# Optimization experiments

Measured on AMD Instinct MI355X. Metric: run time of the kernel, lower is better.

The kernel has to match this reference:

```python
import math
import jax, jax.numpy as jnp
import numpy as np

NUM_BUCKETS = 32
MAX_DISTANCE = 128


def _relative_position_bucket(relative_position):
    # bidirectional=False: positive relative positions map to bucket 0
    rp = -jnp.minimum(relative_position, 0)  # non-negative distances
    max_exact = NUM_BUCKETS // 2
    is_small = rp < max_exact
    # clamp to >=1 before log to avoid log(0); those lanes are selected away by is_small
    rp_large = max_exact + (
        jnp.log(jnp.maximum(rp, 1).astype(jnp.float32) / max_exact)
        / math.log(MAX_DISTANCE / max_exact)
        * (NUM_BUCKETS - max_exact)
    ).astype(jnp.int32)
    rp_large = jnp.minimum(rp_large, NUM_BUCKETS - 1)
    return jnp.where(is_small, rp, rp_large)


def setup_inputs() -> dict:
    key = jax.random.key(0)
    k1, k2, k3, k4 = jax.random.split(key, 4)
    B, L, H, E = 4, 2048, 8, 64
    return {
        "queries": jax.random.normal(k1, (B, L, H, E), dtype=jnp.float32),
        "keys": jax.random.normal(k2, (B, L, H, E), dtype=jnp.float32),
        "values": jax.random.normal(k3, (B, L, H, E), dtype=jnp.float32),
        "bias_table": jax.random.normal(k4, (NUM_BUCKETS, 8), dtype=jnp.float32),
    }


def reference(queries, keys, values, bias_table):
    B, L, H, E = queries.shape
    scale = 1.0 / math.sqrt(E)

    # scores: [B, H, L, S]
    scores = jnp.einsum("blhe,bshe->bhls", queries, keys)

    # causal mask (TriangularCausalMask): masked positions -> -inf BEFORE scaling
    causal = jnp.triu(jnp.ones((L, L), dtype=bool), k=1)  # [L, L]
    scores = jnp.where(causal[None, None], -jnp.inf, scores)

    attn = scale * scores

    # T5-style relative position bias: [1, H, L, L]
    pos = jnp.arange(L)
    rel_pos = pos[None, :] - pos[:, None]  # memory - query
    buckets = _relative_position_bucket(rel_pos)  # [L, L] in [0, 32)
    bias = bias_table[buckets]  # [L, L, 8]
    bias = jnp.transpose(bias, (2, 0, 1))[None]  # [1, 8, L, L]
    attn = attn + bias

    series = jax.nn.softmax(attn, axis=-1)  # dropout p=0.0 -> identity
    V = jnp.einsum("bhls,bshd->blhd", series, values)
    return V
```

## Files before the change

kernel.cpp:

```cpp
#include <hip/hip_runtime.h>
#include <hip/hip_bf16.h>
#include <math.h>

typedef __attribute__((ext_vector_type(8)))  short short8;
typedef __attribute__((ext_vector_type(4)))  float floatx4;
typedef __attribute__((ext_vector_type(16))) float f32x16;

#define L_SEQ 2048
#define NHEADS 8
#define EDIM 64
#define PLANE (L_SEQ * EDIM)
#define LOG2E 1.4426950408889634f

union U8 { unsigned u[4]; short8 s; };

__device__ __forceinline__ unsigned cvt_pk(float lo, float hi) {
    unsigned r;
    asm("v_cvt_pk_bf16_f32 %0, %1, %2" : "=v"(r) : "v"(lo), "v"(hi));
    return r;
}
__device__ __forceinline__ short8 pack8(floatx4 a, floatx4 b) {
    U8 r;
    r.u[0] = cvt_pk(a[0], a[1]); r.u[1] = cvt_pk(a[2], a[3]);
    r.u[2] = cvt_pk(b[0], b[1]); r.u[3] = cvt_pk(b[2], b[3]);
    return r.s;
}
__device__ __forceinline__ unsigned xswap32(unsigned v) {
    return (unsigned)__shfl_xor((int)v, 32);
}

__global__ __launch_bounds__(256) void prep_frag(
    const float* __restrict__ K, const float* __restrict__ V,
    unsigned short* __restrict__ Kf, unsigned short* __restrict__ Vf)
{
    __shared__ unsigned short Tk[64][72];
    __shared__ unsigned short Tv[64][72];
    const int st  = blockIdx.x;
    const int bh  = blockIdx.y;
    const int b   = bh >> 3, h = bh & 7;
    const int tid = threadIdx.x;
    const int sb  = st * 64;

    {
        int s0 = tid >> 3, e0 = (tid & 7) * 8;
        #pragma unroll
        for (int j = 0; j < 2; ++j) {
            int s = s0 + j * 32;
            const float* kp = K + ((size_t)(b * L_SEQ + sb + s) * NHEADS + h) * EDIM + e0;
            floatx4 f0 = *(const floatx4*)kp;
            floatx4 f1 = *(const floatx4*)(kp + 4);
            *(short8*)&Tk[s][e0] = pack8(f0, f1);
        }
    }
    {
        int e = tid & 63, sg = tid >> 6;
        #pragma unroll
        for (int j = 0; j < 16; ++j) {
            int s = sg * 16 + j;
            float v = V[((size_t)(b * L_SEQ + sb + s) * NHEADS + h) * EDIM + e];
            union { float f; unsigned u; } cv; cv.f = v;
            Tv[e][s] = (unsigned short)((cv.u + 0x7FFFu + ((cv.u >> 16) & 1u)) >> 16);
        }
    }
    __syncthreads();
    {
        int s2 = tid >> 7, t7 = tid & 127, ec = t7 >> 5, l31 = t7 & 31;
        #pragma unroll
        for (int hi = 0; hi < 2; ++hi) {
            int row = s2 * 32 + l31, e = ec * 16 + hi * 8;
            short8 v = *(const short8*)&Tk[row][e];
            size_t unit = (((size_t)bh * 64 + st * 2 + s2) * 4 + ec) * 64 + hi * 32 + l31;
            *(short8*)&Kf[unit * 8] = v;
        }
    }
    {
        int s2 = tid >> 7, t7 = tid & 127, et = t7 >> 6, lane = t7 & 63;
        #pragma unroll
        for (int c = 0; c < 2; ++c) {
            int e = et * 32 + (lane & 31), k0 = s2 * 32 + c * 16 + (lane >> 5) * 8;
            short8 v = *(const short8*)&Tv[e][k0];
            size_t unit = ((((size_t)bh * 64 + st * 2 + s2) * 2 + et) * 2 + c) * 64 + lane;
            *(short8*)&Vf[unit * 8] = v;
        }
    }
}

__global__ __launch_bounds__(256, 3) void attn_fwd(
    const float* __restrict__ Q, const unsigned short* __restrict__ Kf,
    const unsigned short* __restrict__ Vf, const float* __restrict__ table,
    float* __restrict__ Out)
{
    __shared__ __align__(16) float bias_lds[L_SEQ];
    __shared__ __align__(16) float osc[2][32][64];
    __shared__ float lsc[2][64];

    const int bid = blockIdx.x;
    const int wid = (bid & 7) * 256 + (bid >> 3);
    const int bh  = wid >> 6;
    const int qg  = 63 - (wid & 63);
    const int b    = bh >> 3, h = bh & 7;
    const int tid  = threadIdx.x;
    const int w    = tid >> 6, lane = tid & 63;
    const int q32  = lane & 31;
    const int hi   = lane >> 5;
    const int hi4  = 4 * hi, hi8 = 8 * hi;
    const int qs   = qg * 32;
    const int qrow = qs + q32;
    const int nsub = qg + 1;

    const int dmax = nsub * 32;
    for (int d = tid; d < dmax; d += 256) {
        int bucket;
        if (d < 16) bucket = d;
        else {
            float t = logf((float)d * 0.0625f) / 2.0794415416798357f * 16.0f;
            int bb = 16 + (int)t;
            bucket = bb < 31 ? bb : 31;
        }
        bias_lds[d] = table[bucket * NHEADS + h] * LOG2E;
    }

    const float* qptr = Q + ((size_t)(b * L_SEQ + qrow) * NHEADS + h) * EDIM;
    short8 qfrag[4];
    #pragma unroll
    for (int ec = 0; ec < 4; ++ec) {
        floatx4 f0 = *(const floatx4*)(qptr + ec * 16 + hi8);
        floatx4 f1 = *(const floatx4*)(qptr + ec * 16 + hi8 + 4);
        qfrag[ec] = pack8(f0, f1);
    }
    __syncthreads();

    const int len = (nsub + 3) >> 2;
    const int r0  = w * len;
    const int r1  = (r0 + len < nsub) ? r0 + len : nsub;

    const unsigned short* kfb = Kf + (size_t)bh * PLANE + lane * 8;
    const unsigned short* vfb = Vf + (size_t)bh * PLANE + lane * 8;

    float  l_run = 0.f;
    f32x16 o_acc[2] = {};

    const float qscale = 0.125f * LOG2E;
    for (int s32 = r0; s32 < r1; ++s32) {
        const bool diag = (s32 == qg);
        const int  kv0s = s32 * 32;

        const unsigned short* kp = kfb + (size_t)s32 * 2048;
        const unsigned short* vp = vfb + (size_t)s32 * 2048;
        short8 kf0 = *(const short8*)(kp);
        short8 kf1 = *(const short8*)(kp + 512);
        short8 kf2 = *(const short8*)(kp + 1024);
        short8 kf3 = *(const short8*)(kp + 1536);
        short8 vf0 = *(const short8*)(vp);
        short8 vf1 = *(const short8*)(vp + 512);
        short8 vf2 = *(const short8*)(vp + 1024);
        short8 vf3 = *(const short8*)(vp + 1536);

        f32x16 st = {};
        __builtin_amdgcn_s_setprio(1);
        st = __builtin_amdgcn_mfma_f32_32x32x16_bf16(kf0, qfrag[0], st, 0, 0, 0);
        st = __builtin_amdgcn_mfma_f32_32x32x16_bf16(kf1, qfrag[1], st, 0, 0, 0);
        st = __builtin_amdgcn_mfma_f32_32x32x16_bf16(kf2, qfrag[2], st, 0, 0, 0);
        st = __builtin_amdgcn_mfma_f32_32x32x16_bf16(kf3, qfrag[3], st, 0, 0, 0);
        __builtin_amdgcn_s_setprio(0);

        float p[16];
        if (!diag) {
            const float* bptr = &bias_lds[qrow - kv0s - hi4];
            #pragma unroll
            for (int r = 0; r < 16; ++r)
                p[r] = exp2f(fmaf(qscale, st[r], bptr[-(r & 3) - 8 * (r >> 2)]));
        } else {
            #pragma unroll
            for (int r = 0; r < 16; ++r) {
                int kidx = (r & 3) + 8 * (r >> 2) + hi4;
                int d = q32 - kidx;
                int dc = d < 0 ? 0 : d;
                float ex = exp2f(fmaf(qscale, st[r], bias_lds[dc]));
                p[r] = (d >= 0) ? ex : 0.0f;
            }
        }

        float s8[8], s4[4], s2[2];
        #pragma unroll
        for (int i = 0; i < 8; ++i) s8[i] = p[2*i] + p[2*i+1];
        #pragma unroll
        for (int i = 0; i < 4; ++i) s4[i] = s8[2*i] + s8[2*i+1];
        s2[0] = s4[0] + s4[1]; s2[1] = s4[2] + s4[3];
        float tsum = s2[0] + s2[1];
        l_run += tsum + __shfl_xor(tsum, 32);

        unsigned a0 = cvt_pk(p[0],  p[1]),  b0 = cvt_pk(p[2],  p[3]);
        unsigned c0 = cvt_pk(p[4],  p[5]),  d0 = cvt_pk(p[6],  p[7]);
        unsigned a1 = cvt_pk(p[8],  p[9]),  b1 = cvt_pk(p[10], p[11]);
        unsigned c1 = cvt_pk(p[12], p[13]), d1 = cvt_pk(p[14], p[15]);
        unsigned as0 = xswap32(a0), bs0 = xswap32(b0);
        unsigned cs0 = xswap32(c0), ds0 = xswap32(d0);
        unsigned as1 = xswap32(a1), bs1 = xswap32(b1);
        unsigned cs1 = xswap32(c1), ds1 = xswap32(d1);
        U8 pf0;
        pf0.u[0] = hi ? cs0 : a0;
        pf0.u[1] = hi ? ds0 : b0;
        pf0.u[2] = hi ? c0  : as0;
        pf0.u[3] = hi ? d0  : bs0;
        U8 pf1;
        pf1.u[0] = hi ? cs1 : a1;
        pf1.u[1] = hi ? ds1 : b1;
        pf1.u[2] = hi ? c1  : as1;
        pf1.u[3] = hi ? d1  : bs1;

        __builtin_amdgcn_s_setprio(1);
        o_acc[0] = __builtin_amdgcn_mfma_f32_32x32x16_bf16(pf0.s, vf0, o_acc[0], 0, 0, 0);
        o_acc[0] = __builtin_amdgcn_mfma_f32_32x32x16_bf16(pf1.s, vf1, o_acc[0], 0, 0, 0);
        o_acc[1] = __builtin_amdgcn_mfma_f32_32x32x16_bf16(pf0.s, vf2, o_acc[1], 0, 0, 0);
        o_acc[1] = __builtin_amdgcn_mfma_f32_32x32x16_bf16(pf1.s, vf3, o_acc[1], 0, 0, 0);
        __builtin_amdgcn_s_setprio(0);
    }

    __syncthreads();
    if (w & 1) {
        int slot = w >> 1;
        #pragma unroll
        for (int et = 0; et < 2; ++et)
            #pragma unroll
            for (int r = 0; r < 16; ++r)
                osc[slot][et * 16 + r][lane] = o_acc[et][r];
        lsc[slot][lane] = l_run;
    }
    __syncthreads();
    if (!(w & 1)) {
        int slot = w >> 1;
        l_run += lsc[slot][lane];
        #pragma unroll
        for (int et = 0; et < 2; ++et)
            #pragma unroll
            for (int r = 0; r < 16; ++r)
                o_acc[et][r] += osc[slot][et * 16 + r][lane];
    }
    __syncthreads();
    if (w == 2) {
        #pragma unroll
        for (int et = 0; et < 2; ++et)
            #pragma unroll
            for (int r = 0; r < 16; ++r)
                osc[0][et * 16 + r][lane] = o_acc[et][r];
        lsc[0][lane] = l_run;
    }
    __syncthreads();
    if (w == 0) {
        l_run += lsc[0][lane];
        #pragma unroll
        for (int et = 0; et < 2; ++et)
            #pragma unroll
            for (int r = 0; r < 16; ++r)
                o_acc[et][r] += osc[0][et * 16 + r][lane];

        float inv = 1.0f / l_run;
        #pragma unroll
        for (int r = 0; r < 16; ++r) {
            int qv = (r & 3) + 8 * (r >> 2) + hi4;
            float iv = __shfl(inv, qv);
            float* op = Out + ((size_t)(b * L_SEQ + qs + qv) * NHEADS + h) * EDIM + q32;
            op[0]  = o_acc[0][r] * iv;
            op[32] = o_acc[1][r] * iv;
        }
    }
}

extern "C" void kernel_launch(void* const* d_in, const int* in_sizes, int n_in,
                              void* d_out, int out_size, void* d_ws, size_t ws_size,
                              hipStream_t stream) {
    const float* Q     = (const float*)d_in[0];
    const float* K     = (const float*)d_in[1];
    const float* V     = (const float*)d_in[2];
    const float* table = (const float*)d_in[3];
    float* Out = (float*)d_out;
    unsigned short* Kf = (unsigned short*)d_ws;
    unsigned short* Vf = Kf + (size_t)4 * NHEADS * PLANE;
    (void)in_sizes; (void)n_in; (void)out_size; (void)ws_size;

    dim3 pgrid(32, 32);
    prep_frag<<<pgrid, 256, 0, stream>>>(K, V, Kf, Vf);
    attn_fwd<<<dim3(2048), 256, 0, stream>>>(Q, Kf, Vf, table, Out);
}
```

Measured before the change: 58.47 us.

## Compute softmax row sums via MFMA with ones and use permlane32 swap

Replaces the scalar tree reduction and cross-half shuffle of the softmax denominator with two extra MFMAs that multiply the bf16 probability fragments by a ones matrix, so row sums land in the same layout as the output accumulator. It also replaces the eight ds_swizzle/shfl_xor exchanges plus selects with four v_permlane32_swap instructions to build the P fragments. The final normalization no longer needs a lane shuffle. The trade-offs are extra matrix work per tile and more accumulator registers, and the denominator is now summed from bf16-rounded probabilities.

New measurement: 58.75 us. Within noise of the previous version (+0.5%).

```diff
diff --git a/kernel.cpp b/kernel.cpp
--- a/kernel.cpp
+++ b/kernel.cpp
@@ -24,9 +24,6 @@
     r.u[0] = cvt_pk(a[0], a[1]); r.u[1] = cvt_pk(a[2], a[3]);
     r.u[2] = cvt_pk(b[0], b[1]); r.u[3] = cvt_pk(b[2], b[3]);
     return r.s;
-}
-__device__ __forceinline__ unsigned xswap32(unsigned v) {
-    return (unsigned)__shfl_xor((int)v, 32);
 }
 
 __global__ __launch_bounds__(256) void prep_frag(
@@ -92,7 +89,7 @@
 {
     __shared__ __align__(16) float bias_lds[L_SEQ];
     __shared__ __align__(16) float osc[2][32][64];
-    __shared__ float lsc[2][64];
+    __shared__ float lsc[2][2][16];
 
     const int bid = blockIdx.x;
     const int wid = (bid & 7) * 256 + (bid >> 3);
@@ -137,8 +134,12 @@
     const unsigned short* kfb = Kf + (size_t)bh * PLANE + lane * 8;
     const unsigned short* vfb = Vf + (size_t)bh * PLANE + lane * 8;
 
-    float  l_run = 0.f;
+    U8 onesf;
+    onesf.u[0] = 0x3F803F80u; onesf.u[1] = 0x3F803F80u;
+    onesf.u[2] = 0x3F803F80u; onesf.u[3] = 0x3F803F80u;
+
     f32x16 o_acc[2] = {};
+    f32x16 o_l = {};
 
     const float qscale = 0.125f * LOG2E;
     for (int s32 = r0; s32 < r1; ++s32) {
@@ -181,39 +182,26 @@
             }
         }
 
-        float s8[8], s4[4], s2[2];
-        #pragma unroll
-        for (int i = 0; i < 8; ++i) s8[i] = p[2*i] + p[2*i+1];
-        #pragma unroll
-        for (int i = 0; i < 4; ++i) s4[i] = s8[2*i] + s8[2*i+1];
-        s2[0] = s4[0] + s4[1]; s2[1] = s4[2] + s4[3];
-        float tsum = s2[0] + s2[1];
-        l_run += tsum + __shfl_xor(tsum, 32);
-
-        unsigned a0 = cvt_pk(p[0],  p[1]),  b0 = cvt_pk(p[2],  p[3]);
-        unsigned c0 = cvt_pk(p[4],  p[5]),  d0 = cvt_pk(p[6],  p[7]);
-        unsigned a1 = cvt_pk(p[8],  p[9]),  b1 = cvt_pk(p[10], p[11]);
-        unsigned c1 = cvt_pk(p[12], p[13]), d1 = cvt_pk(p[14], p[15]);
-        unsigned as0 = xswap32(a0), bs0 = xswap32(b0);
-        unsigned cs0 = xswap32(c0), ds0 = xswap32(d0);
-        unsigned as1 = xswap32(a1), bs1 = xswap32(b1);
-        unsigned cs1 = xswap32(c1), ds1 = xswap32(d1);
+        unsigned x0 = cvt_pk(p[0],  p[1]),  x1 = cvt_pk(p[2],  p[3]);
+        unsigned y0 = cvt_pk(p[4],  p[5]),  y1 = cvt_pk(p[6],  p[7]);
+        unsigned x2 = cvt_pk(p[8],  p[9]),  x3 = cvt_pk(p[10], p[11]);
+        unsigned y2 = cvt_pk(p[12], p[13]), y3 = cvt_pk(p[14], p[15]);
+        asm("v_permlane32_swap_b32 %0, %1" : "+v"(x0), "+v"(y0));
+        asm("v_permlane32_swap_b32 %0, %1" : "+v"(x1), "+v"(y1));
+        asm("v_permlane32_swap_b32 %0, %1" : "+v"(x2), "+v"(y2));
+        asm("v_permlane32_swap_b32 %0, %1" : "+v"(x3), "+v"(y3));
         U8 pf0;
-        pf0.u[0] = hi ? cs0 : a0;
-        pf0.u[1] = hi ? ds0 : b0;
-        pf0.u[2] = hi ? c0  : as0;
-        pf0.u[3] = hi ? d0  : bs0;
+        pf0.u[0] = x0; pf0.u[1] = x1; pf0.u[2] = y0; pf0.u[3] = y1;
         U8 pf1;
-        pf1.u[0] = hi ? cs1 : a1;
-        pf1.u[1] = hi ? ds1 : b1;
-        pf1.u[2] = hi ? c1  : as1;
-        pf1.u[3] = hi ? d1  : bs1;
+        pf1.u[0] = x2; pf1.u[1] = x3; pf1.u[2] = y2; pf1.u[3] = y3;
 
         __builtin_amdgcn_s_setprio(1);
         o_acc[0] = __builtin_amdgcn_mfma_f32_32x32x16_bf16(pf0.s, vf0, o_acc[0], 0, 0, 0);
         o_acc[0] = __builtin_amdgcn_mfma_f32_32x32x16_bf16(pf1.s, vf1, o_acc[0], 0, 0, 0);
         o_acc[1] = __builtin_amdgcn_mfma_f32_32x32x16_bf16(pf0.s, vf2, o_acc[1], 0, 0, 0);
         o_acc[1] = __builtin_amdgcn_mfma_f32_32x32x16_bf16(pf1.s, vf3, o_acc[1], 0, 0, 0);
+        o_l      = __builtin_amdgcn_mfma_f32_32x32x16_bf16(pf0.s, onesf.s, o_l, 0, 0, 0);
+        o_l      = __builtin_amdgcn_mfma_f32_32x32x16_bf16(pf1.s, onesf.s, o_l, 0, 0, 0);
         __builtin_amdgcn_s_setprio(0);
     }
 
@@ -225,17 +213,21 @@
             #pragma unroll
             for (int r = 0; r < 16; ++r)
                 osc[slot][et * 16 + r][lane] = o_acc[et][r];
-        lsc[slot][lane] = l_run;
+        if (q32 == 0) {
+            #pragma unroll
+            for (int r = 0; r < 16; ++r) lsc[slot][hi][r] = o_l[r];
+        }
     }
     __syncthreads();
     if (!(w & 1)) {
         int slot = w >> 1;
-        l_run += lsc[slot][lane];
         #pragma unroll
         for (int et = 0; et < 2; ++et)
             #pragma unroll
             for (int r = 0; r < 16; ++r)
                 o_acc[et][r] += osc[slot][et * 16 + r][lane];
+        #pragma unroll
+        for (int r = 0; r < 16; ++r) o_l[r] += lsc[slot][hi][r];
     }
     __syncthreads();
     if (w == 2) {
@@ -244,22 +236,25 @@
             #pragma unroll
             for (int r = 0; r < 16; ++r)
                 osc[0][et * 16 + r][lane] = o_acc[et][r];
-        lsc[0][lane] = l_run;
+        if (q32 == 0) {
+            #pragma unroll
+            for (int r = 0; r < 16; ++r) lsc[0][hi][r] = o_l[r];
+        }
     }
     __syncthreads();
     if (w == 0) {
-        l_run += lsc[0][lane];
         #pragma unroll
         for (int et = 0; et < 2; ++et)
             #pragma unroll
             for (int r = 0; r < 16; ++r)
                 o_acc[et][r] += osc[0][et * 16 + r][lane];
-
-        float inv = 1.0f / l_run;
+        #pragma unroll
+        for (int r = 0; r < 16; ++r) o_l[r] += lsc[0][hi][r];
+
         #pragma unroll
         for (int r = 0; r < 16; ++r) {
             int qv = (r & 3) + 8 * (r >> 2) + hi4;
-            float iv = __shfl(inv, qv);
+            float iv = 1.0f / o_l[r];
             float* op = Out + ((size_t)(b * L_SEQ + qs + qv) * NHEADS + h) * EDIM + q32;
             op[0]  = o_acc[0][r] * iv;
             op[32] = o_acc[1][r] * iv;
```
